# Optimization experiments

Hardware: AMD Instinct MI355X
Metric: run time of the kernel (lower is better)

## Reference

```python
import jax, jax.numpy as jnp
import numpy as np

DILATION = 512
C_RES = 128
C_SKIP = 256


def setup_inputs() -> dict:
    key = jax.random.key(0)
    ks = jax.random.split(key, 6)
    B, T = 8, 16384
    x = jax.random.normal(ks[0], (B, C_RES, T), dtype=jnp.float32)
    # dilated conv weight: [out_ch, in_ch, kernel=2], no bias
    w_dil = jax.random.normal(ks[1], (C_RES, C_RES, 2), dtype=jnp.float32) * (1.0 / np.sqrt(2 * C_RES))
    # 1x1 residual conv (with bias)
    w_res = jax.random.normal(ks[2], (C_RES, C_RES), dtype=jnp.float32) * (1.0 / np.sqrt(C_RES))
    b_res = jax.random.normal(ks[3], (C_RES,), dtype=jnp.float32) * 0.01
    # 1x1 skip conv (with bias)
    w_skip = jax.random.normal(ks[4], (C_SKIP, C_RES), dtype=jnp.float32) * (1.0 / np.sqrt(C_RES))
    b_skip = jax.random.normal(ks[5], (C_SKIP,), dtype=jnp.float32) * 0.01
    return {"x": x, "w_dil": w_dil, "w_res": w_res, "b_res": b_res,
            "w_skip": w_skip, "b_skip": b_skip, "skip_size": 4096}


def reference(x, w_dil, w_res, b_res, w_skip, b_skip, skip_size):
    # x: [B, C, T]. Dilated causal conv, kernel_size=2, dilation=DILATION, no padding:
    # pre[:, :, t] = W[:,:,0] @ x[:,:,t] + W[:,:,1] @ x[:,:,t+DILATION], t in [0, T-DILATION)
    T = x.shape[2]
    L = T - DILATION  # output length
    pre = (jnp.einsum('oi,bit->bot', w_dil[:, :, 0], x[:, :, :L]) +
           jnp.einsum('oi,bit->bot', w_dil[:, :, 1], x[:, :, DILATION:]))
    activated = jnp.tanh(pre) * jax.nn.sigmoid(pre)  # filter * gate
    # 1x1 residual conv + residual add with the time-aligned tail of x
    out = (jnp.einsum('oi,bit->bot', w_res, activated) + b_res[None, :, None]
           + x[:, :, T - L:])
    # 1x1 skip conv, keep last skip_size steps
    skip = jnp.einsum('oi,bit->bot', w_skip, activated) + b_skip[None, :, None]
    skip = skip[:, :, -skip_size:]
    return (out, skip)
```

## Files before the change

### kernel.cpp

```cpp
#include <hip/hip_runtime.h>

typedef float f32x4 __attribute__((ext_vector_type(4)));
typedef __bf16 bf16x8 __attribute__((ext_vector_type(8)));

__device__ __forceinline__ unsigned short f2bf(float f) {
  unsigned u = __builtin_bit_cast(unsigned, f);
  u = (u + 0x7FFFu + ((u >> 16) & 1u)) >> 16;
  return (unsigned short)u;
}

__device__ __forceinline__ f32x4 MFMA16(uint4 a, uint4 b, f32x4 c) {
  return __builtin_amdgcn_mfma_f32_16x16x32_bf16(
      __builtin_bit_cast(bf16x8, a), __builtin_bit_cast(bf16x8, b), c, 0, 0, 0);
}

__global__ void wn_prep(const float* __restrict__ wd, const float* __restrict__ wres,
                        const float* __restrict__ wskip, unsigned short* __restrict__ ws16) {
  int g = blockIdx.x * 256 + threadIdx.x;
  if (g < 32768) {
    int kc = g >> 12, rem = g & 4095;
    int o = rem >> 5, kl = rem & 31;
    int k = kc * 32 + kl;
    int tap = k >> 7, i = k & 127;
    ws16[g] = f2bf(wd[(o << 8) + (i << 1) + tap]);
  } else {
    int g2 = g - 32768;
    int pkk = g2 >> 12;
    int rem = g2 & 4095;
    int o = rem >> 5, kl = rem & 31;
    int p = pkk >> 2, kk = pkk & 3;
    int k = kk * 32 + kl;
    float v = (p == 0) ? wres[o * 128 + k] : wskip[((p - 1) * 128 + o) * 128 + k];
    ws16[32768 + g2] = f2bf(v);
  }
}

__global__ __launch_bounds__(256, 4) void wn_main(
    const float* __restrict__ x,
    const float* __restrict__ bres_g,
    const float* __restrict__ bskip_g,
    const unsigned short* __restrict__ wd2_img,
    const unsigned short* __restrict__ wrs2_img,
    float* __restrict__ out,
    float* __restrict__ skipo) {
  __shared__ unsigned short actT[64 * 140];

  const int w = blockIdx.x;
  const int b = w & 7;
  const int tile = 247 - (w >> 3);
  const int t0 = tile * 64;

  const int tid = threadIdx.x;
  const int lane = tid & 63;
  const int wv = tid >> 6;
  const int mw = wv >> 1;
  const int nw = wv & 1;
  const int l15 = lane & 15;
  const int lhi = lane >> 4;

  const float* xb_base = x + (size_t)b * (128 * 16384);

  f32x4 acc[4][2];
#pragma unroll
  for (int i = 0; i < 4; ++i)
#pragma unroll
    for (int j = 0; j < 2; ++j) acc[i][j] = (f32x4){0.f, 0.f, 0.f, 0.f};

  const float* xcol = xb_base + t0 + nw * 32 + l15;
#pragma unroll 2
  for (int kc = 0; kc < 8; ++kc) {
    uint4 af[4];
    const unsigned short* wbase = wd2_img + (kc << 12) + lhi * 8;
#pragma unroll
    for (int mi = 0; mi < 4; ++mi)
      af[mi] = *(const uint4*)(wbase + (mw * 64 + mi * 16 + l15) * 32);
    const float* xq = xcol + (size_t)((kc & 3) * 32 + lhi * 8) * 16384 + (kc >> 2) * 512;
    float xf[2][8];
#pragma unroll
    for (int ni = 0; ni < 2; ++ni)
#pragma unroll
      for (int j = 0; j < 8; ++j)
        xf[ni][j] = xq[(size_t)j * 16384 + ni * 16];
    uint4 bfr[2];
#pragma unroll
    for (int ni = 0; ni < 2; ++ni) {
      bf16x8 t;
#pragma unroll
      for (int j = 0; j < 8; ++j) t[j] = (__bf16)xf[ni][j];
      bfr[ni] = __builtin_bit_cast(uint4, t);
    }
#pragma unroll
    for (int mi = 0; mi < 4; ++mi)
#pragma unroll
      for (int ni = 0; ni < 2; ++ni)
        acc[mi][ni] = MFMA16(af[mi], bfr[ni], acc[mi][ni]);
  }

#pragma unroll
  for (int mi = 0; mi < 4; ++mi) {
#pragma unroll
    for (int ni = 0; ni < 2; ++ni) {
      ushort4 av;
#pragma unroll
      for (int r = 0; r < 4; ++r) {
        float p = acc[mi][ni][r];
        p = fminf(fmaxf(p, -15.f), 15.f);
        float ep = __expf(p);
        float e2 = ep * ep;
        float sg = ep * __builtin_amdgcn_rcpf(1.f + ep);
        float th = (e2 - 1.f) * __builtin_amdgcn_rcpf(e2 + 1.f);
        ((unsigned short*)&av)[r] = f2bf(th * sg);
      }
      int trow = nw * 32 + ni * 16 + l15;
      int o0 = mw * 64 + mi * 16 + lhi * 4;
      *(ushort4*)(actT + trow * 140 + o0) = av;
    }
  }
  __syncthreads();

  const int npass = (tile >= 184) ? 3 : 1;
  for (int p = 0; p < npass; ++p) {
    f32x4 acc2[4][2];
#pragma unroll
    for (int i = 0; i < 4; ++i)
#pragma unroll
      for (int j = 0; j < 2; ++j) acc2[i][j] = (f32x4){0.f, 0.f, 0.f, 0.f};

#pragma unroll
    for (int kk = 0; kk < 4; ++kk) {
      uint4 af[4], bfr[2];
      const unsigned short* wbase = wrs2_img + ((p * 4 + kk) << 12) + lhi * 8;
#pragma unroll
      for (int mi = 0; mi < 4; ++mi)
        af[mi] = *(const uint4*)(wbase + (mw * 64 + mi * 16 + l15) * 32);
#pragma unroll
      for (int ni = 0; ni < 2; ++ni)
        bfr[ni] = *(const uint4*)(actT + (nw * 32 + ni * 16 + l15) * 140 + kk * 32 + lhi * 8);
#pragma unroll
      for (int mi = 0; mi < 4; ++mi)
#pragma unroll
        for (int ni = 0; ni < 2; ++ni)
          acc2[mi][ni] = MFMA16(af[mi], bfr[ni], acc2[mi][ni]);
    }

    if (p == 0) {
#pragma unroll
      for (int mi = 0; mi < 4; ++mi) {
        int o0 = mw * 64 + mi * 16 + lhi * 4;
        float br[4];
#pragma unroll
        for (int r = 0; r < 4; ++r) br[r] = bres_g[o0 + r];
#pragma unroll
        for (int ni = 0; ni < 2; ++ni) {
          int tl = nw * 32 + ni * 16 + l15;
#pragma unroll
          for (int r = 0; r < 4; ++r) {
            size_t row = (size_t)(b * 128 + o0 + r);
            float v = acc2[mi][ni][r] + br[r] + x[row * 16384 + 512 + t0 + tl];
            out[row * 15872 + t0 + tl] = v;
          }
        }
      }
    } else {
#pragma unroll
      for (int mi = 0; mi < 4; ++mi) {
        int o2 = (p - 1) * 128 + mw * 64 + mi * 16 + lhi * 4;
        float bs[4];
#pragma unroll
        for (int r = 0; r < 4; ++r) bs[r] = bskip_g[o2 + r];
#pragma unroll
        for (int ni = 0; ni < 2; ++ni) {
          int tl = nw * 32 + ni * 16 + l15;
          int s = t0 + tl - 11776;
#pragma unroll
          for (int r = 0; r < 4; ++r) {
            skipo[(size_t)(b * 256 + o2 + r) * 4096 + s] = acc2[mi][ni][r] + bs[r];
          }
        }
      }
    }
  }
}

extern "C" void kernel_launch(void* const* d_in, const int* in_sizes, int n_in,
                              void* d_out, int out_size, void* d_ws, size_t ws_size,
                              hipStream_t stream) {
  const float* x      = (const float*)d_in[0];
  const float* w_dil  = (const float*)d_in[1];
  const float* w_res  = (const float*)d_in[2];
  const float* b_res  = (const float*)d_in[3];
  const float* w_skip = (const float*)d_in[4];
  const float* b_skip = (const float*)d_in[5];
  unsigned short* ws16 = (unsigned short*)d_ws;
  float* out = (float*)d_out;
  float* skipo = out + 16252928;

  wn_prep<<<320, 256, 0, stream>>>(w_dil, w_res, w_skip, ws16);

  wn_main<<<1984, 256, 0, stream>>>(x, b_res, b_skip, ws16, ws16 + 32768, out, skipo);
}
```

Before: 95.41 us.

## Stage x tile through double-buffered LDS with cooperative vector loads

Replaces the per-lane strided scalar global loads of x (eight rows per lane, each 64KB apart) with a cooperative float2 load pattern. Each thread converts its values to bf16 and writes them into a double-buffered LDS tile, and the MFMA B-fragments are then read from LDS. The load of the next k-chunk is issued before the current chunk's MFMAs, overlapping global latency with compute. In exchange it adds a __syncthreads per k-chunk and switches to dynamic shared memory, and several loops are de-unrolled (unroll 1), which may reduce ILP.

```diff
diff --git a/kernel.cpp b/kernel.cpp
--- a/kernel.cpp
+++ b/kernel.cpp
@@ -43,7 +43,9 @@
     const unsigned short* __restrict__ wrs2_img,
     float* __restrict__ out,
     float* __restrict__ skipo) {
-  __shared__ unsigned short actT[64 * 140];
+  extern __shared__ unsigned short lds[];
+  unsigned short* xls  = lds;
+  unsigned short* actT = lds;
 
   const int w = blockIdx.x;
   const int b = w & 7;
@@ -58,42 +60,64 @@
   const int l15 = lane & 15;
   const int lhi = lane >> 4;
 
+  const int kq = tid & 7;
+  const int tpr = tid >> 3;
+
   const float* xb_base = x + (size_t)b * (128 * 16384);
 
+  float2 xr[4];
+
+  auto issueX = [&](int kc) {
+    int kglob = kc * 32 + kq * 4;
+    int tap = kglob >> 7;
+    int ib = kglob & 127;
+    const float* p = xb_base + (size_t)ib * 16384 + (t0 + tap * 512 + tpr * 2);
+    xr[0] = *(const float2*)(p);
+    xr[1] = *(const float2*)(p + 16384);
+    xr[2] = *(const float2*)(p + 32768);
+    xr[3] = *(const float2*)(p + 49152);
+  };
+  auto writeX = [&](int buf) {
+    unsigned short* dst = xls + buf * 2560;
+    int r0 = tpr * 2;
+    ushort4 a0, a1;
+    a0.x = f2bf(xr[0].x); a0.y = f2bf(xr[1].x); a0.z = f2bf(xr[2].x); a0.w = f2bf(xr[3].x);
+    a1.x = f2bf(xr[0].y); a1.y = f2bf(xr[1].y); a1.z = f2bf(xr[2].y); a1.w = f2bf(xr[3].y);
+    *(ushort4*)(dst + r0 * 40 + kq * 4) = a0;
+    *(ushort4*)(dst + (r0 + 1) * 40 + kq * 4) = a1;
+  };
+
   f32x4 acc[4][2];
 #pragma unroll
   for (int i = 0; i < 4; ++i)
 #pragma unroll
     for (int j = 0; j < 2; ++j) acc[i][j] = (f32x4){0.f, 0.f, 0.f, 0.f};
 
-  const float* xcol = xb_base + t0 + nw * 32 + l15;
-#pragma unroll 2
+  issueX(0);
+  writeX(0);
+  __syncthreads();
+
+#pragma unroll 1
   for (int kc = 0; kc < 8; ++kc) {
+    const int buf = kc & 1;
+    if (kc < 7) issueX(kc + 1);
     uint4 af[4];
     const unsigned short* wbase = wd2_img + (kc << 12) + lhi * 8;
 #pragma unroll
     for (int mi = 0; mi < 4; ++mi)
       af[mi] = *(const uint4*)(wbase + (mw * 64 + mi * 16 + l15) * 32);
-    const float* xq = xcol + (size_t)((kc & 3) * 32 + lhi * 8) * 16384 + (kc >> 2) * 512;
-    float xf[2][8];
+    uint4 bfr[2];
+    const unsigned short* xbuf = xls + buf * 2560;
 #pragma unroll
     for (int ni = 0; ni < 2; ++ni)
-#pragma unroll
-      for (int j = 0; j < 8; ++j)
-        xf[ni][j] = xq[(size_t)j * 16384 + ni * 16];
-    uint4 bfr[2];
-#pragma unroll
-    for (int ni = 0; ni < 2; ++ni) {
-      bf16x8 t;
-#pragma unroll
-      for (int j = 0; j < 8; ++j) t[j] = (__bf16)xf[ni][j];
-      bfr[ni] = __builtin_bit_cast(uint4, t);
-    }
+      bfr[ni] = *(const uint4*)(xbuf + (nw * 32 + ni * 16 + l15) * 40 + lhi * 8);
 #pragma unroll
     for (int mi = 0; mi < 4; ++mi)
 #pragma unroll
       for (int ni = 0; ni < 2; ++ni)
         acc[mi][ni] = MFMA16(af[mi], bfr[ni], acc[mi][ni]);
+    if (kc < 7) writeX(buf ^ 1);
+    __syncthreads();
   }
 
 #pragma unroll
@@ -119,6 +143,7 @@
   __syncthreads();
 
   const int npass = (tile >= 184) ? 3 : 1;
+#pragma unroll 1
   for (int p = 0; p < npass; ++p) {
     f32x4 acc2[4][2];
 #pragma unroll
@@ -126,7 +151,7 @@
 #pragma unroll
       for (int j = 0; j < 2; ++j) acc2[i][j] = (f32x4){0.f, 0.f, 0.f, 0.f};
 
-#pragma unroll
+#pragma unroll 1
     for (int kk = 0; kk < 4; ++kk) {
       uint4 af[4], bfr[2];
       const unsigned short* wbase = wrs2_img + ((p * 4 + kk) << 12) + lhi * 8;
@@ -197,5 +222,5 @@
 
   wn_prep<<<320, 256, 0, stream>>>(w_dil, w_res, w_skip, ws16);
 
-  wn_main<<<1984, 256, 0, stream>>>(x, b_res, b_skip, ws16, ws16 + 32768, out, skipo);
-}
+  wn_main<<<1984, 256, 17920, stream>>>(x, b_res, b_skip, ws16, ws16 + 32768, out, skipo);
+}
```

New measurement: 89.34 us. -6.4%, faster.

## Stage x tile cooperatively into LDS as bf16 before dilated-conv MFMA

Applied to the files above, without the earlier changes.

All threads first load the block's input slice with coalesced float2 global loads, convert to bf16, and store it in a padded LDS buffer. The MFMA loop then reads B fragments from LDS instead of issuing strided scalar global loads that were duplicated across waves. The activation buffer aliases the same dynamic LDS, and an extra barrier keeps the two uses apart. LDS per block grows to 36 KB, which may constrain occupancy, and the residual/skip loops get reduced unrolling.

```diff
diff --git a/kernel.cpp b/kernel.cpp
--- a/kernel.cpp
+++ b/kernel.cpp
@@ -43,7 +43,9 @@
     const unsigned short* __restrict__ wrs2_img,
     float* __restrict__ out,
     float* __restrict__ skipo) {
-  __shared__ unsigned short actT[64 * 140];
+  extern __shared__ unsigned short lds[];
+  unsigned short* xall = lds;
+  unsigned short* actT = lds;
 
   const int w = blockIdx.x;
   const int b = w & 7;
@@ -58,15 +60,48 @@
   const int l15 = lane & 15;
   const int lhi = lane >> 4;
 
+  const int kq = tid & 7;
+  const int tpr = tid >> 3;
+
   const float* xb_base = x + (size_t)b * (128 * 16384);
 
+  float2 xr[4][4];
+
+  auto issueX = [&](int kc, int s) {
+    int kglob = kc * 32 + kq * 4;
+    int tap = kglob >> 7;
+    int ib = kglob & 127;
+    const float* p = xb_base + (size_t)ib * 16384 + (t0 + tap * 512 + tpr * 2);
+    xr[s][0] = *(const float2*)(p);
+    xr[s][1] = *(const float2*)(p + 16384);
+    xr[s][2] = *(const float2*)(p + 32768);
+    xr[s][3] = *(const float2*)(p + 49152);
+  };
+  auto writeX = [&](int kc, int s) {
+    unsigned short* dst = xall + kc * 2304;
+    int r0 = tpr * 2;
+    ushort4 a0, a1;
+    a0.x = f2bf(xr[s][0].x); a0.y = f2bf(xr[s][1].x); a0.z = f2bf(xr[s][2].x); a0.w = f2bf(xr[s][3].x);
+    a1.x = f2bf(xr[s][0].y); a1.y = f2bf(xr[s][1].y); a1.z = f2bf(xr[s][2].y); a1.w = f2bf(xr[s][3].y);
+    *(ushort4*)(dst + r0 * 36 + kq * 4) = a0;
+    *(ushort4*)(dst + (r0 + 1) * 36 + kq * 4) = a1;
+  };
+
   f32x4 acc[4][2];
 #pragma unroll
   for (int i = 0; i < 4; ++i)
 #pragma unroll
     for (int j = 0; j < 2; ++j) acc[i][j] = (f32x4){0.f, 0.f, 0.f, 0.f};
 
-  const float* xcol = xb_base + t0 + nw * 32 + l15;
+#pragma unroll
+  for (int half = 0; half < 2; ++half) {
+#pragma unroll
+    for (int c = 0; c < 4; ++c) issueX(half * 4 + c, c);
+#pragma unroll
+    for (int c = 0; c < 4; ++c) writeX(half * 4 + c, c);
+  }
+  __syncthreads();
+
 #pragma unroll 2
   for (int kc = 0; kc < 8; ++kc) {
     uint4 af[4];
@@ -74,27 +109,18 @@
 #pragma unroll
     for (int mi = 0; mi < 4; ++mi)
       af[mi] = *(const uint4*)(wbase + (mw * 64 + mi * 16 + l15) * 32);
-    const float* xq = xcol + (size_t)((kc & 3) * 32 + lhi * 8) * 16384 + (kc >> 2) * 512;
-    float xf[2][8];
+    uint4 bfr[2];
+    const unsigned short* xbuf = xall + kc * 2304;
 #pragma unroll
     for (int ni = 0; ni < 2; ++ni)
-#pragma unroll
-      for (int j = 0; j < 8; ++j)
-        xf[ni][j] = xq[(size_t)j * 16384 + ni * 16];
-    uint4 bfr[2];
-#pragma unroll
-    for (int ni = 0; ni < 2; ++ni) {
-      bf16x8 t;
-#pragma unroll
-      for (int j = 0; j < 8; ++j) t[j] = (__bf16)xf[ni][j];
-      bfr[ni] = __builtin_bit_cast(uint4, t);
-    }
+      bfr[ni] = *(const uint4*)(xbuf + (nw * 32 + ni * 16 + l15) * 36 + lhi * 8);
 #pragma unroll
     for (int mi = 0; mi < 4; ++mi)
 #pragma unroll
       for (int ni = 0; ni < 2; ++ni)
         acc[mi][ni] = MFMA16(af[mi], bfr[ni], acc[mi][ni]);
   }
+  __syncthreads();
 
 #pragma unroll
   for (int mi = 0; mi < 4; ++mi) {
@@ -119,6 +145,7 @@
   __syncthreads();
 
   const int npass = (tile >= 184) ? 3 : 1;
+#pragma unroll 1
   for (int p = 0; p < npass; ++p) {
     f32x4 acc2[4][2];
 #pragma unroll
@@ -126,7 +153,7 @@
 #pragma unroll
       for (int j = 0; j < 2; ++j) acc2[i][j] = (f32x4){0.f, 0.f, 0.f, 0.f};
 
-#pragma unroll
+#pragma unroll 2
     for (int kk = 0; kk < 4; ++kk) {
       uint4 af[4], bfr[2];
       const unsigned short* wbase = wrs2_img + ((p * 4 + kk) << 12) + lhi * 8;
@@ -197,5 +224,5 @@
 
   wn_prep<<<320, 256, 0, stream>>>(w_dil, w_res, w_skip, ws16);
 
-  wn_main<<<1984, 256, 0, stream>>>(x, b_res, b_skip, ws16, ws16 + 32768, out, skipo);
-}
+  wn_main<<<1984, 256, 36864, stream>>>(x, b_res, b_skip, ws16, ws16 + 32768, out, skipo);
+}
```

Measured after the change: 91.65 us. -3.9%, faster.

## Give each wave its own 16-column time slice to drop block barrier

Applied to the files above, without the earlier changes.

Work is re-split so each of the four waves owns 16 time columns and all 128 output channels, instead of a 2x2 split of channels and time. The activation tile is kept in a per-wave LDS region, so the __syncthreads between the gated activation and the residual/skip GEMMs goes away. In exchange every wave now reads the full weight matrices, which doubles weight traffic through cache. Each wave also issues one x fragment per k-step instead of two, which lowers memory-level parallelism per wave.

```diff
diff --git a/kernel.cpp b/kernel.cpp
--- a/kernel.cpp
+++ b/kernel.cpp
@@ -43,7 +43,7 @@
     const unsigned short* __restrict__ wrs2_img,
     float* __restrict__ out,
     float* __restrict__ skipo) {
-  __shared__ unsigned short actT[64 * 140];
+  __shared__ unsigned short actLds[4][16 * 136];
 
   const int w = blockIdx.x;
   const int b = w & 7;
@@ -53,129 +53,107 @@
   const int tid = threadIdx.x;
   const int lane = tid & 63;
   const int wv = tid >> 6;
-  const int mw = wv >> 1;
-  const int nw = wv & 1;
   const int l15 = lane & 15;
   const int lhi = lane >> 4;
+  const int t0w = t0 + wv * 16;
+
+  unsigned short* actw = &actLds[wv][0];
 
   const float* xb_base = x + (size_t)b * (128 * 16384);
 
-  f32x4 acc[4][2];
+  f32x4 acc[8];
 #pragma unroll
-  for (int i = 0; i < 4; ++i)
-#pragma unroll
-    for (int j = 0; j < 2; ++j) acc[i][j] = (f32x4){0.f, 0.f, 0.f, 0.f};
+  for (int i = 0; i < 8; ++i) acc[i] = (f32x4){0.f, 0.f, 0.f, 0.f};
 
-  const float* xcol = xb_base + t0 + nw * 32 + l15;
 #pragma unroll 2
   for (int kc = 0; kc < 8; ++kc) {
+    const float* xq = xb_base + (size_t)((kc & 3) * 32 + lhi * 8) * 16384
+                    + t0w + ((kc >> 2) << 9) + l15;
+    float xf[8];
+#pragma unroll
+    for (int j = 0; j < 8; ++j) xf[j] = xq[(size_t)j * 16384];
+    const unsigned short* wbase = wd2_img + (kc << 12) + lhi * 8;
     uint4 af[4];
-    const unsigned short* wbase = wd2_img + (kc << 12) + lhi * 8;
+    bf16x8 tv;
+#pragma unroll
+    for (int j = 0; j < 8; ++j) tv[j] = (__bf16)xf[j];
+    uint4 bfr = __builtin_bit_cast(uint4, tv);
 #pragma unroll
     for (int mi = 0; mi < 4; ++mi)
-      af[mi] = *(const uint4*)(wbase + (mw * 64 + mi * 16 + l15) * 32);
-    const float* xq = xcol + (size_t)((kc & 3) * 32 + lhi * 8) * 16384 + (kc >> 2) * 512;
-    float xf[2][8];
-#pragma unroll
-    for (int ni = 0; ni < 2; ++ni)
-#pragma unroll
-      for (int j = 0; j < 8; ++j)
-        xf[ni][j] = xq[(size_t)j * 16384 + ni * 16];
-    uint4 bfr[2];
-#pragma unroll
-    for (int ni = 0; ni < 2; ++ni) {
-      bf16x8 t;
-#pragma unroll
-      for (int j = 0; j < 8; ++j) t[j] = (__bf16)xf[ni][j];
-      bfr[ni] = __builtin_bit_cast(uint4, t);
-    }
+      af[mi] = *(const uint4*)(wbase + (mi * 16 + l15) * 32);
 #pragma unroll
     for (int mi = 0; mi < 4; ++mi)
+      acc[mi] = MFMA16(af[mi], bfr, acc[mi]);
 #pragma unroll
-      for (int ni = 0; ni < 2; ++ni)
-        acc[mi][ni] = MFMA16(af[mi], bfr[ni], acc[mi][ni]);
+    for (int mi = 0; mi < 4; ++mi)
+      af[mi] = *(const uint4*)(wbase + ((mi + 4) * 16 + l15) * 32);
+#pragma unroll
+    for (int mi = 0; mi < 4; ++mi)
+      acc[mi + 4] = MFMA16(af[mi], bfr, acc[mi + 4]);
   }
 
 #pragma unroll
-  for (int mi = 0; mi < 4; ++mi) {
+  for (int mi = 0; mi < 8; ++mi) {
+    ushort4 av;
 #pragma unroll
-    for (int ni = 0; ni < 2; ++ni) {
-      ushort4 av;
-#pragma unroll
-      for (int r = 0; r < 4; ++r) {
-        float p = acc[mi][ni][r];
-        p = fminf(fmaxf(p, -15.f), 15.f);
-        float ep = __expf(p);
-        float e2 = ep * ep;
-        float sg = ep * __builtin_amdgcn_rcpf(1.f + ep);
-        float th = (e2 - 1.f) * __builtin_amdgcn_rcpf(e2 + 1.f);
-        ((unsigned short*)&av)[r] = f2bf(th * sg);
-      }
-      int trow = nw * 32 + ni * 16 + l15;
-      int o0 = mw * 64 + mi * 16 + lhi * 4;
-      *(ushort4*)(actT + trow * 140 + o0) = av;
+    for (int r = 0; r < 4; ++r) {
+      float p = acc[mi][r];
+      p = fminf(fmaxf(p, -15.f), 15.f);
+      float ep = __expf(p);
+      float e2 = ep * ep;
+      float sg = ep * __builtin_amdgcn_rcpf(1.f + ep);
+      float th = (e2 - 1.f) * __builtin_amdgcn_rcpf(e2 + 1.f);
+      ((unsigned short*)&av)[r] = f2bf(th * sg);
     }
+    *(ushort4*)(actw + l15 * 136 + mi * 16 + lhi * 4) = av;
   }
-  __syncthreads();
 
   const int npass = (tile >= 184) ? 3 : 1;
+#pragma unroll 1
   for (int p = 0; p < npass; ++p) {
-    f32x4 acc2[4][2];
+    f32x4 acc2[8];
 #pragma unroll
-    for (int i = 0; i < 4; ++i)
-#pragma unroll
-      for (int j = 0; j < 2; ++j) acc2[i][j] = (f32x4){0.f, 0.f, 0.f, 0.f};
+    for (int i = 0; i < 8; ++i) acc2[i] = (f32x4){0.f, 0.f, 0.f, 0.f};
 
-#pragma unroll
+#pragma unroll 2
     for (int kk = 0; kk < 4; ++kk) {
-      uint4 af[4], bfr[2];
+      uint4 bfr = *(const uint4*)(actw + l15 * 136 + kk * 32 + lhi * 8);
       const unsigned short* wbase = wrs2_img + ((p * 4 + kk) << 12) + lhi * 8;
+      uint4 af[4];
 #pragma unroll
       for (int mi = 0; mi < 4; ++mi)
-        af[mi] = *(const uint4*)(wbase + (mw * 64 + mi * 16 + l15) * 32);
-#pragma unroll
-      for (int ni = 0; ni < 2; ++ni)
-        bfr[ni] = *(const uint4*)(actT + (nw * 32 + ni * 16 + l15) * 140 + kk * 32 + lhi * 8);
+        af[mi] = *(const uint4*)(wbase + (mi * 16 + l15) * 32);
 #pragma unroll
       for (int mi = 0; mi < 4; ++mi)
+        acc2[mi] = MFMA16(af[mi], bfr, acc2[mi]);
 #pragma unroll
-        for (int ni = 0; ni < 2; ++ni)
-          acc2[mi][ni] = MFMA16(af[mi], bfr[ni], acc2[mi][ni]);
+      for (int mi = 0; mi < 4; ++mi)
+        af[mi] = *(const uint4*)(wbase + ((mi + 4) * 16 + l15) * 32);
+#pragma unroll
+      for (int mi = 0; mi < 4; ++mi)
+        acc2[mi + 4] = MFMA16(af[mi], bfr, acc2[mi + 4]);
     }
 
     if (p == 0) {
 #pragma unroll
-      for (int mi = 0; mi < 4; ++mi) {
-        int o0 = mw * 64 + mi * 16 + lhi * 4;
-        float br[4];
+      for (int mi = 0; mi < 8; ++mi) {
+        int o0 = mi * 16 + lhi * 4;
+        int tl = t0w + l15;
 #pragma unroll
-        for (int r = 0; r < 4; ++r) br[r] = bres_g[o0 + r];
-#pragma unroll
-        for (int ni = 0; ni < 2; ++ni) {
-          int tl = nw * 32 + ni * 16 + l15;
-#pragma unroll
-          for (int r = 0; r < 4; ++r) {
-            size_t row = (size_t)(b * 128 + o0 + r);
-            float v = acc2[mi][ni][r] + br[r] + x[row * 16384 + 512 + t0 + tl];
-            out[row * 15872 + t0 + tl] = v;
-          }
+        for (int r = 0; r < 4; ++r) {
+          size_t row = (size_t)(b * 128 + o0 + r);
+          float v = acc2[mi][r] + bres_g[o0 + r] + x[row * 16384 + 512 + tl];
+          out[row * 15872 + tl] = v;
         }
       }
     } else {
 #pragma unroll
-      for (int mi = 0; mi < 4; ++mi) {
-        int o2 = (p - 1) * 128 + mw * 64 + mi * 16 + lhi * 4;
-        float bs[4];
+      for (int mi = 0; mi < 8; ++mi) {
+        int o2 = (p - 1) * 128 + mi * 16 + lhi * 4;
+        int s = t0w + l15 - 11776;
 #pragma unroll
-        for (int r = 0; r < 4; ++r) bs[r] = bskip_g[o2 + r];
-#pragma unroll
-        for (int ni = 0; ni < 2; ++ni) {
-          int tl = nw * 32 + ni * 16 + l15;
-          int s = t0 + tl - 11776;
-#pragma unroll
-          for (int r = 0; r < 4; ++r) {
-            skipo[(size_t)(b * 256 + o2 + r) * 4096 + s] = acc2[mi][ni][r] + bs[r];
-          }
+        for (int r = 0; r < 4; ++r) {
+          skipo[(size_t)(b * 256 + o2 + r) * 4096 + s] = acc2[mi][r] + bskip_g[o2 + r];
         }
       }
     }
```

After: 115.7 us. 1.21x slower.
